# Optimization experiments

Hardware: AMD Instinct MI355X
Metric: run time of the kernel (lower is better)

Reference implementation:

```python
import jax, jax.numpy as jnp
import numpy as np

B, N, M = 4, 8192, 8192


def setup_inputs() -> dict:
    key = jax.random.key(0)
    k1, k2, k3, k4 = jax.random.split(key, 4)
    xyz1 = jax.random.normal(k1, (B, N, 3), dtype=jnp.float32)
    xyz2 = jax.random.normal(k2, (B, M, 3), dtype=jnp.float32)
    weights1 = jax.random.uniform(k3, (B, N), dtype=jnp.float32)
    weights2 = jax.random.uniform(k4, (B, M), dtype=jnp.float32)
    return {"xyz1": xyz1, "xyz2": xyz2, "weights1": weights1, "weights2": weights2}


def _chamfer_dists(xyz1, xyz2):
    # Squared L2 pairwise distances via the ||a||^2 + ||b||^2 - 2 a.b identity
    # (avoids materializing a [B, N, M, 3] difference tensor).
    sq1 = jnp.sum(xyz1 * xyz1, axis=-1)            # [B, N]
    sq2 = jnp.sum(xyz2 * xyz2, axis=-1)            # [B, M]
    dots = jnp.einsum("bnc,bmc->bnm", xyz1, xyz2)  # [B, N, M]
    d = sq1[:, :, None] + sq2[:, None, :] - 2.0 * dots
    d = jnp.maximum(d, 0.0)
    dist1 = jnp.min(d, axis=2)  # [B, N] nearest in xyz2 for each point in xyz1
    dist2 = jnp.min(d, axis=1)  # [B, M] nearest in xyz1 for each point in xyz2
    return dist1, dist2


def reference(xyz1, xyz2, weights1, weights2):
    dist1, dist2 = _chamfer_dists(xyz1, xyz2)
    dist1 = dist1 * weights1
    dist2 = dist2 * weights2
    dist1_avg = jnp.sum(dist1) / jnp.sum(weights1)
    dist2_avg = jnp.sum(dist2) / jnp.sum(weights2)
    return (dist1_avg + dist2_avg) / 2.0
```

## Files before the change

kernel.cpp:

```cpp
#include <hip/hip_runtime.h>

#define TPB 256
constexpr int Bsz  = 4;
constexpr int Npts = 8192;
constexpr int Mpts = 8192;
constexpr int PTS  = Bsz * Npts;
constexpr int QT_PER_B = Npts / 16;
constexpr int CT_PER_B = Mpts / 16;
constexpr int RBLK = 64;

typedef __attribute__((ext_vector_type(8))) short short8;
typedef __attribute__((ext_vector_type(4))) float f32x4;

__device__ __forceinline__ float min3f(float a, float b, float c) {
    return fminf(fminf(a, b), c);
}

__device__ __forceinline__ void mfma4_bf16(const short8& a0, const short8& a1,
                                           const short8& a2, const short8& a3,
                                           const short8& b,
                                           f32x4& d0, f32x4& d1,
                                           f32x4& d2, f32x4& d3) {
    asm("v_mfma_f32_16x16x32_bf16 %0, %4, %8, 0\n\t"
        "v_mfma_f32_16x16x32_bf16 %1, %5, %8, 0\n\t"
        "v_mfma_f32_16x16x32_bf16 %2, %6, %8, 0\n\t"
        "v_mfma_f32_16x16x32_bf16 %3, %7, %8, 0\n\t"
        "s_nop 7\n\t"
        "s_nop 3"
        : "=&v"(d0), "=&v"(d1), "=&v"(d2), "=&v"(d3)
        : "v"(a0), "v"(a1), "v"(a2), "v"(a3), "v"(b));
}

__device__ __forceinline__ unsigned short bfh(float v) {
    unsigned u = __float_as_uint(v);
    return (unsigned short)((u + 0x7fffu + ((u >> 16) & 1u)) >> 16);
}
__device__ __forceinline__ float b2f(unsigned short h) {
    return __uint_as_float(((unsigned)h) << 16);
}
__device__ __forceinline__ void split3(float v, unsigned short& h,
                                       unsigned short& m, unsigned short& l) {
    h = bfh(v); float fh = b2f(h);
    m = bfh(v - fh); float fm = b2f(m);
    l = bfh(v - fh - fm);
}

__device__ __forceinline__ unsigned short pickA(int o, unsigned short h,
                                                unsigned short m, unsigned short l) {
    return o < 3 ? h : (o < 5 ? m : l);
}
__device__ __forceinline__ unsigned short pickB(int o, unsigned short h,
                                                unsigned short m, unsigned short l) {
    return (o == 1 || o == 4) ? m : (o == 2 ? l : h);
}

__global__ void __launch_bounds__(TPB) prep_kernel(
    const float* __restrict__ xyz1, const float* __restrict__ xyz2,
    short* __restrict__ aQ, short* __restrict__ bC)
{
    int id   = blockIdx.x * TPB + threadIdx.x;
    int side = id >> 17;
    int tl   = id & 131071;
    int tile = tl >> 6, lane = tl & 63;
    int r = lane & 15, g = lane >> 4;

    const float* src = side ? xyz2 : xyz1;
    int p = tile * 16 + r;
    float x = src[p * 3 + 0], y = src[p * 3 + 1], z = src[p * 3 + 2];
    float n = fmaf(x, x, fmaf(y, y, z * z));
    float s = side ? 1.f : -2.f;

    unsigned short xh, xm, xl, yh, ym, yl, zh, zm, zl, nh, nm, nl;
    split3(s * x, xh, xm, xl);
    split3(s * y, yh, ym, yl);
    split3(s * z, zh, zm, zl);
    split3(n, nh, nm, nl);
    const unsigned short ONE = 0x3F80;

    short8 v;
#pragma unroll
    for (int j = 0; j < 8; ++j) {
        int k = g * 8 + j;
        unsigned short u = 0;
        if (k < 18) {
            int c = k / 6, o = k - 6 * c;
            unsigned short h = c == 0 ? xh : (c == 1 ? yh : zh);
            unsigned short m = c == 0 ? xm : (c == 1 ? ym : zm);
            unsigned short l = c == 0 ? xl : (c == 1 ? yl : zl);
            u = side ? pickB(o, h, m, l) : pickA(o, h, m, l);
        } else if (k < 21) {
            u = side ? ONE : (k == 18 ? nh : (k == 19 ? nm : nl));
        } else if (k < 24) {
            u = side ? (k == 21 ? nh : (k == 22 ? nm : nl)) : ONE;
        }
        v[j] = (short)u;
    }
    short8* dst = (short8*)(side ? bC : aQ);
    dst[tile * 64 + lane] = v;
}

__global__ void __launch_bounds__(TPB, 4) chamfer_mfma_kernel(
    const short* __restrict__ aQ, const short* __restrict__ bC,
    unsigned int* __restrict__ partials)
{
    int bid = blockIdx.x;
    int linear = (bid & 7) * 128 + (bid >> 3);
    int batch = linear >> 8;
    int rem = linear & 255;
    int qs = rem >> 3;
    int cs = rem & 7;
    int w = threadIdx.x >> 6, lane = threadIdx.x & 63;

    int qtile0 = batch * QT_PER_B + qs * 16 + w * 4;
    int ctile0 = batch * CT_PER_B + cs * 64;

    const short8* aT = (const short8*)aQ;
    const short8* bT = (const short8*)bC;

    __shared__ unsigned int colb[1024];
#pragma unroll
    for (int i = 0; i < 4; ++i)
        colb[threadIdx.x + i * 256] = 0x7f7fffffu;

    short8 afrag[4];
#pragma unroll
    for (int t = 0; t < 4; ++t) afrag[t] = aT[(qtile0 + t) * 64 + lane];

    const f32x4 inf4 = {3.4e38f, 3.4e38f, 3.4e38f, 3.4e38f};
    f32x4 rowp[4];
#pragma unroll
    for (int t = 0; t < 4; ++t) rowp[t] = inf4;
    __syncthreads();

    const short8* bP = bT + ctile0 * 64 + lane;
    unsigned int* mycol = &colb[lane & 15];

#pragma unroll 4
    for (int ct = 0; ct < 64; ++ct) {
        short8 bf = bP[ct * 64];

        f32x4 d0, d1, d2, d3;
        mfma4_bf16(afrag[0], afrag[1], afrag[2], afrag[3], bf, d0, d1, d2, d3);

        rowp[0] = __builtin_elementwise_min(rowp[0], d0);
        rowp[1] = __builtin_elementwise_min(rowp[1], d1);
        rowp[2] = __builtin_elementwise_min(rowp[2], d2);
        rowp[3] = __builtin_elementwise_min(rowp[3], d3);

        float ca = min3f(d0[0], d0[1], d0[2]);
        ca = min3f(ca, d0[3], d1[0]);
        ca = min3f(ca, d1[1], d1[2]);
        ca = fminf(ca, d1[3]);
        float cb = min3f(d2[0], d2[1], d2[2]);
        cb = min3f(cb, d2[3], d3[0]);
        cb = min3f(cb, d3[1], d3[2]);
        cb = fminf(cb, d3[3]);
        atomicMin(mycol + ct * 16, __float_as_uint(fmaxf(fminf(ca, cb), 0.f)));
    }

#pragma unroll
    for (int t = 0; t < 4; ++t) {
#pragma unroll
        for (int i = 0; i < 4; ++i) {
            float v = rowp[t][i];
            v = fminf(v, __shfl_xor(v, 1));
            v = fminf(v, __shfl_xor(v, 2));
            v = fminf(v, __shfl_xor(v, 4));
            v = fminf(v, __shfl_xor(v, 8));
            if ((lane & 15) == 0) {
                int q = (qtile0 + t) * 16 + (lane >> 4) * 4 + i;
                atomicMin(&partials[q], __float_as_uint(fmaxf(v, 0.f)));
            }
        }
    }

    __syncthreads();
    int cbase = PTS + ctile0 * 16;
#pragma unroll
    for (int i = 0; i < 4; ++i)
        atomicMin(&partials[cbase + threadIdx.x + i * 256],
                  colb[threadIdx.x + i * 256]);
}

__global__ void __launch_bounds__(TPB) reduce_kernel(
    const float* __restrict__ partials,
    const float* __restrict__ w1, const float* __restrict__ w2,
    float2* __restrict__ slots)
{
    int gid = blockIdx.x * TPB + threadIdx.x;
    int dir = gid >> 13;
    int idx = gid & 8191;
    const float4* d4 = (const float4*)(partials + (size_t)dir * PTS);
    const float4* w4 = (const float4*)(dir ? w2 : w1);
    float4 d = d4[idx], w = w4[idx];
    float c = d.x * w.x + d.y * w.y + d.z * w.z + d.w * w.w;
    float s = w.x + w.y + w.z + w.w;

    for (int off = 32; off; off >>= 1) {
        c += __shfl_down(c, off);
        s += __shfl_down(s, off);
    }
    __shared__ float sc[4], ss[4];
    int lane = threadIdx.x & 63, wid = threadIdx.x >> 6;
    if (lane == 0) { sc[wid] = c; ss[wid] = s; }
    __syncthreads();
    if (threadIdx.x == 0) {
        slots[blockIdx.x] =
            make_float2(sc[0] + sc[1] + sc[2] + sc[3],
                        ss[0] + ss[1] + ss[2] + ss[3]);
    }
}

__global__ void __launch_bounds__(64) final_kernel(
    const float2* __restrict__ slots, float* __restrict__ out)
{
    float2 v = slots[threadIdx.x];
    for (int off = 16; off; off >>= 1) {
        v.x += __shfl_down(v.x, off, 32);
        v.y += __shfl_down(v.y, off, 32);
    }
    float c1 = __shfl(v.x, 32), s1 = __shfl(v.y, 32);
    if (threadIdx.x == 0)
        out[0] = 0.5f * (v.x / v.y + c1 / s1);
}

extern "C" void kernel_launch(void* const* d_in, const int* in_sizes, int n_in,
                              void* d_out, int out_size, void* d_ws, size_t ws_size,
                              hipStream_t stream) {
    const float* xyz1 = (const float*)d_in[0];
    const float* xyz2 = (const float*)d_in[1];
    const float* w1   = (const float*)d_in[2];
    const float* w2   = (const float*)d_in[3];
    float* out = (float*)d_out;

    unsigned int* partials = (unsigned int*)d_ws;
    float2* slots = (float2*)((char*)d_ws + (size_t)2 * PTS * sizeof(unsigned int));
    short* aQ = (short*)((char*)d_ws + (1u << 20));
    short* bC = (short*)((char*)d_ws + (4u << 20));

    prep_kernel<<<1024, TPB, 0, stream>>>(xyz1, xyz2, aQ, bC);
    chamfer_mfma_kernel<<<1024, TPB, 0, stream>>>(aQ, bC, partials);
    reduce_kernel<<<RBLK, TPB, 0, stream>>>((const float*)partials, w1, w2, slots);
    final_kernel<<<1, 64, 0, stream>>>(slots, out);
}
```

Measured before the change: 105.2 us.

## Split chamfer block into eight waves with two query tiles each and prefetch B

The chamfer kernel now launches 512-thread blocks. Each of the eight waves owns two query tiles instead of four, so the block still covers the same 16x64 tile region. The B fragment for the next column tile is loaded one step ahead, a manual software prefetch. The aim is to cut per-wave register pressure and raise the number of resident waves to hide MFMA and load latency. The cost is twice as many LDS column atomicMin operations and B-fragment loads per block, since each wave now reduces only two tiles before issuing its atomic.

```diff
diff --git a/kernel.cpp b/kernel.cpp
--- a/kernel.cpp
+++ b/kernel.cpp
@@ -1,6 +1,7 @@
 #include <hip/hip_runtime.h>
 
 #define TPB 256
+#define TPBM 512
 constexpr int Bsz  = 4;
 constexpr int Npts = 8192;
 constexpr int Mpts = 8192;
@@ -16,19 +17,15 @@
     return fminf(fminf(a, b), c);
 }
 
-__device__ __forceinline__ void mfma4_bf16(const short8& a0, const short8& a1,
-                                           const short8& a2, const short8& a3,
+__device__ __forceinline__ void mfma2_bf16(const short8& a0, const short8& a1,
                                            const short8& b,
-                                           f32x4& d0, f32x4& d1,
-                                           f32x4& d2, f32x4& d3) {
-    asm("v_mfma_f32_16x16x32_bf16 %0, %4, %8, 0\n\t"
-        "v_mfma_f32_16x16x32_bf16 %1, %5, %8, 0\n\t"
-        "v_mfma_f32_16x16x32_bf16 %2, %6, %8, 0\n\t"
-        "v_mfma_f32_16x16x32_bf16 %3, %7, %8, 0\n\t"
+                                           f32x4& d0, f32x4& d1) {
+    asm("v_mfma_f32_16x16x32_bf16 %0, %2, %4, 0\n\t"
+        "v_mfma_f32_16x16x32_bf16 %1, %3, %4, 0\n\t"
         "s_nop 7\n\t"
         "s_nop 3"
-        : "=&v"(d0), "=&v"(d1), "=&v"(d2), "=&v"(d3)
-        : "v"(a0), "v"(a1), "v"(a2), "v"(a3), "v"(b));
+        : "=&v"(d0), "=&v"(d1)
+        : "v"(a0), "v"(a1), "v"(b));
 }
 
 __device__ __forceinline__ unsigned short bfh(float v) {
@@ -99,7 +96,7 @@
     dst[tile * 64 + lane] = v;
 }
 
-__global__ void __launch_bounds__(TPB, 4) chamfer_mfma_kernel(
+__global__ void __launch_bounds__(TPBM, 8) chamfer_mfma_kernel(
     const short* __restrict__ aQ, const short* __restrict__ bC,
     unsigned int* __restrict__ partials)
 {
@@ -111,58 +108,62 @@
     int cs = rem & 7;
     int w = threadIdx.x >> 6, lane = threadIdx.x & 63;
 
-    int qtile0 = batch * QT_PER_B + qs * 16 + w * 4;
+    int qtile0 = batch * QT_PER_B + qs * 16 + w * 2;
     int ctile0 = batch * CT_PER_B + cs * 64;
 
     const short8* aT = (const short8*)aQ;
     const short8* bT = (const short8*)bC;
 
     __shared__ unsigned int colb[1024];
-#pragma unroll
-    for (int i = 0; i < 4; ++i)
-        colb[threadIdx.x + i * 256] = 0x7f7fffffu;
-
-    short8 afrag[4];
-#pragma unroll
-    for (int t = 0; t < 4; ++t) afrag[t] = aT[(qtile0 + t) * 64 + lane];
+    colb[threadIdx.x]       = 0x7f7fffffu;
+    colb[threadIdx.x + 512] = 0x7f7fffffu;
+
+    short8 a0 = aT[(qtile0 + 0) * 64 + lane];
+    short8 a1 = aT[(qtile0 + 1) * 64 + lane];
 
     const f32x4 inf4 = {3.4e38f, 3.4e38f, 3.4e38f, 3.4e38f};
-    f32x4 rowp[4];
-#pragma unroll
-    for (int t = 0; t < 4; ++t) rowp[t] = inf4;
+    f32x4 rowp0 = inf4, rowp1 = inf4;
     __syncthreads();
 
     const short8* bP = bT + ctile0 * 64 + lane;
     unsigned int* mycol = &colb[lane & 15];
 
-#pragma unroll 4
-    for (int ct = 0; ct < 64; ++ct) {
-        short8 bf = bP[ct * 64];
-
-        f32x4 d0, d1, d2, d3;
-        mfma4_bf16(afrag[0], afrag[1], afrag[2], afrag[3], bf, d0, d1, d2, d3);
-
-        rowp[0] = __builtin_elementwise_min(rowp[0], d0);
-        rowp[1] = __builtin_elementwise_min(rowp[1], d1);
-        rowp[2] = __builtin_elementwise_min(rowp[2], d2);
-        rowp[3] = __builtin_elementwise_min(rowp[3], d3);
-
-        float ca = min3f(d0[0], d0[1], d0[2]);
-        ca = min3f(ca, d0[3], d1[0]);
-        ca = min3f(ca, d1[1], d1[2]);
-        ca = fminf(ca, d1[3]);
-        float cb = min3f(d2[0], d2[1], d2[2]);
-        cb = min3f(cb, d2[3], d3[0]);
-        cb = min3f(cb, d3[1], d3[2]);
-        cb = fminf(cb, d3[3]);
-        atomicMin(mycol + ct * 16, __float_as_uint(fmaxf(fminf(ca, cb), 0.f)));
+    short8 b0 = bP[0], b1;
+
+#pragma unroll 2
+    for (int ct = 0; ct < 64; ct += 2) {
+        b1 = bP[(ct + 1) * 64];
+        {
+            f32x4 d0, d1;
+            mfma2_bf16(a0, a1, b0, d0, d1);
+            rowp0 = __builtin_elementwise_min(rowp0, d0);
+            rowp1 = __builtin_elementwise_min(rowp1, d1);
+            float ca = min3f(d0[0], d0[1], d0[2]);
+            ca = min3f(ca, d0[3], d1[0]);
+            ca = min3f(ca, d1[1], d1[2]);
+            ca = fminf(ca, d1[3]);
+            atomicMin(mycol + ct * 16, __float_as_uint(fmaxf(ca, 0.f)));
+        }
+        b0 = bP[(ct + 2) * 64];
+        {
+            f32x4 d0, d1;
+            mfma2_bf16(a0, a1, b1, d0, d1);
+            rowp0 = __builtin_elementwise_min(rowp0, d0);
+            rowp1 = __builtin_elementwise_min(rowp1, d1);
+            float ca = min3f(d0[0], d0[1], d0[2]);
+            ca = min3f(ca, d0[3], d1[0]);
+            ca = min3f(ca, d1[1], d1[2]);
+            ca = fminf(ca, d1[3]);
+            atomicMin(mycol + (ct + 1) * 16, __float_as_uint(fmaxf(ca, 0.f)));
+        }
     }
 
 #pragma unroll
-    for (int t = 0; t < 4; ++t) {
+    for (int t = 0; t < 2; ++t) {
+        f32x4 rp = t ? rowp1 : rowp0;
 #pragma unroll
         for (int i = 0; i < 4; ++i) {
-            float v = rowp[t][i];
+            float v = rp[i];
             v = fminf(v, __shfl_xor(v, 1));
             v = fminf(v, __shfl_xor(v, 2));
             v = fminf(v, __shfl_xor(v, 4));
@@ -176,10 +177,8 @@
 
     __syncthreads();
     int cbase = PTS + ctile0 * 16;
-#pragma unroll
-    for (int i = 0; i < 4; ++i)
-        atomicMin(&partials[cbase + threadIdx.x + i * 256],
-                  colb[threadIdx.x + i * 256]);
+    atomicMin(&partials[cbase + threadIdx.x],       colb[threadIdx.x]);
+    atomicMin(&partials[cbase + threadIdx.x + 512], colb[threadIdx.x + 512]);
 }
 
 __global__ void __launch_bounds__(TPB) reduce_kernel(
@@ -239,7 +238,7 @@
     short* bC = (short*)((char*)d_ws + (4u << 20));
 
     prep_kernel<<<1024, TPB, 0, stream>>>(xyz1, xyz2, aQ, bC);
-    chamfer_mfma_kernel<<<1024, TPB, 0, stream>>>(aQ, bC, partials);
+    chamfer_mfma_kernel<<<1024, TPBM, 0, stream>>>(aQ, bC, partials);
     reduce_kernel<<<RBLK, TPB, 0, stream>>>((const float*)partials, w1, w2, slots);
     final_kernel<<<1, 64, 0, stream>>>(slots, out);
 }
```

After: 94.88 us. 1.11x faster.
